# Optimization experiments

Hardware: AMD Instinct MI355X
Metric: run time of the kernel (lower is better)

Reference implementation:

```python
import jax, jax.numpy as jnp
import numpy as np

EPS_LN = 1e-5
EPS_ACT = 1e-5
EPS_W = 1e-8


def _layer_norm(x):
    # F.layer_norm(x, [d]) with no affine params, eps=1e-5, biased variance
    mu = jnp.mean(x, axis=-1, keepdims=True)
    xc = x - mu
    var = jnp.mean(xc * xc, axis=-1, keepdims=True)
    return xc * jax.lax.rsqrt(var + EPS_LN)


def _activation_quant(x):
    # per-token absmax int8 fake-quant (dequantized back to float)
    scale = 127.0 / jnp.clip(jnp.max(jnp.abs(x), axis=-1, keepdims=True), EPS_ACT)
    return jnp.clip(jnp.round(x * scale), -128, 127) / scale


def _weight_quant(w):
    # ternary {-1,0,+1} absmean quantization, rescaled by absmean
    scale = jnp.clip(jnp.mean(jnp.abs(w)), EPS_W)
    return jnp.clip(jnp.round(w / scale), -1, 1) * scale


def _bitlinear(x, w, b):
    xn = _layer_norm(x)
    xq = _activation_quant(xn)        # forward value (STE irrelevant for fwd)
    wq = _weight_quant(w)
    return jnp.einsum('bsd,fd->bsf', xq, wq) + b


def setup_inputs() -> dict:
    key = jax.random.key(0)
    k1, k2, k3, k4, k5 = jax.random.split(key, 5)
    d_model, d_ff = 2048, 8192
    B, S = 4, 2048
    x = jax.random.normal(k1, (B, S, d_model), dtype=jnp.float32)
    # nn.Linear default init: U(-1/sqrt(fan_in), 1/sqrt(fan_in))
    lim1 = 1.0 / np.sqrt(d_model)
    lim2 = 1.0 / np.sqrt(d_ff)
    w1 = jax.random.uniform(k2, (d_ff, d_model), jnp.float32, -lim1, lim1)
    b1 = jax.random.uniform(k3, (d_ff,), jnp.float32, -lim1, lim1)
    w2 = jax.random.uniform(k4, (d_model, d_ff), jnp.float32, -lim2, lim2)
    b2 = jax.random.uniform(k5, (d_model,), jnp.float32, -lim2, lim2)
    return {"x": x, "w1": w1, "b1": b1, "w2": w2, "b2": b2}


def reference(x, w1, b1, w2, b2):
    h = _bitlinear(x, w1, b1)
    h = jax.nn.gelu(h, approximate=False)  # torch F.gelu default = exact erf
    # dropout p=0.0 -> identity
    return _bitlinear(h, w2, b2)
```

## Files before the change

### kernel.cpp

```cpp
#include <hip/hip_runtime.h>

typedef int     i32x4 __attribute__((ext_vector_type(4)));
typedef _Float16 f16x2 __attribute__((ext_vector_type(2)));

__device__ __forceinline__ void async_cp16(const void* g, void* l) {
    __builtin_amdgcn_global_load_lds(
        (const __attribute__((address_space(1))) void*)g,
        (__attribute__((address_space(3))) void*)l, 16, 0, 0);
}

template <bool GELU, typename OutT>
__global__ __launch_bounds__(256) void gemm_i8(
    const signed char* __restrict__ A,
    const signed char* __restrict__ B,
    const float* __restrict__ rowinv,
    const float* __restrict__ wscale,
    const float* __restrict__ bias,
    OutT* __restrict__ C,
    int M, int N, int K)
{
    __shared__ signed char sA[128 * 128];
    __shared__ signed char sB[128 * 128];

    const int tid  = threadIdx.x;
    const int lane = tid & 63;
    const int wid  = tid >> 6;
    const int lm   = lane & 15;
    const int quad = lane >> 4;
    const int wr   = (wid >> 1) * 64;
    const int wc   = (wid & 1) * 64;

    const long long rowA0 = (long long)blockIdx.y * 128;
    const long long rowB0 = (long long)blockIdx.x * 128;

    const int srow   = tid >> 3;
    const int slot   = tid & 7;
    const int gchunk = slot ^ (srow & 7);

    const signed char* aP = A + (rowA0 + srow) * (long long)K + gchunk * 16;
    const signed char* bP = B + (rowB0 + srow) * (long long)K + gchunk * 16;
    signed char* sA_t = &sA[tid * 16];
    signed char* sB_t = &sB[tid * 16];
    const long long rstep = 32LL * K;

    i32x4 acc[4][4] = {};

    const int swz = lm & 7;

    for (int k0 = 0; k0 < K; k0 += 128) {
#pragma unroll
        for (int r = 0; r < 4; ++r) {
            async_cp16(aP + r * rstep + k0, sA_t + r * 4096);
            async_cp16(bP + r * rstep + k0, sB_t + r * 4096);
        }
        __syncthreads();
#pragma unroll
        for (int ks = 0; ks < 2; ++ks) {
            const int coff = ((ks * 4 + quad) ^ swz) * 16;
            i32x4 af[4], bfr[4];
#pragma unroll
            for (int i = 0; i < 4; ++i)
                af[i] = *(const i32x4*)&sA[(wr + i * 16 + lm) * 128 + coff];
#pragma unroll
            for (int j = 0; j < 4; ++j)
                bfr[j] = *(const i32x4*)&sB[(wc + j * 16 + lm) * 128 + coff];
#pragma unroll
            for (int i = 0; i < 4; ++i)
#pragma unroll
                for (int j = 0; j < 4; ++j)
                    acc[i][j] = __builtin_amdgcn_mfma_i32_16x16x64_i8(
                        af[i], bfr[j], acc[i][j], 0, 0, 0);
        }
        __syncthreads();
    }

    const float sw = wscale[0];
    float bj[4];
#pragma unroll
    for (int j = 0; j < 4; ++j)
        bj[j] = bias[rowB0 + wc + j * 16 + lm];

#pragma unroll
    for (int i = 0; i < 4; ++i) {
#pragma unroll
        for (int r = 0; r < 4; ++r) {
            const long long gr = rowA0 + wr + i * 16 + quad * 4 + r;
            const float rs = sw * rowinv[gr];
#pragma unroll
            for (int j = 0; j < 4; ++j) {
                const long long gc = rowB0 + wc + j * 16 + lm;
                float v = (float)acc[i][j][r] * rs + bj[j];
                if constexpr (GELU)
                    v = 0.5f * v * (1.0f + erff(v * 0.70710678118654752f));
                C[gr * (long long)N + gc] = (OutT)v;
            }
        }
    }
}

__global__ __launch_bounds__(256) void ln_quant_x(
    const float* __restrict__ x, signed char* __restrict__ xq,
    float* __restrict__ xinv)
{
    const int t = blockIdx.x;
    const int tid = threadIdx.x;
    const int lane = tid & 63, wid = tid >> 6;
    const float4* row = (const float4*)(x + (long long)t * 2048);
    float4 v0 = row[tid];
    float4 v1 = row[tid + 256];
    float vv[8] = {v0.x, v0.y, v0.z, v0.w, v1.x, v1.y, v1.z, v1.w};

    float s = 0.f, mn = vv[0], mx = vv[0];
#pragma unroll
    for (int i = 0; i < 8; ++i) { s += vv[i]; mn = fminf(mn, vv[i]); mx = fmaxf(mx, vv[i]); }
#pragma unroll
    for (int off = 32; off > 0; off >>= 1) {
        s += __shfl_down(s, off);
        mn = fminf(mn, __shfl_down(mn, off));
        mx = fmaxf(mx, __shfl_down(mx, off));
    }
    __shared__ float rS[4], rMn[4], rMx[4];
    if (lane == 0) { rS[wid] = s; rMn[wid] = mn; rMx[wid] = mx; }
    __syncthreads();
    s  = rS[0] + rS[1] + rS[2] + rS[3];
    mn = fminf(fminf(rMn[0], rMn[1]), fminf(rMn[2], rMn[3]));
    mx = fmaxf(fmaxf(rMx[0], rMx[1]), fmaxf(rMx[2], rMx[3]));
    const float mu = s * (1.0f / 2048.0f);

    float ssc = 0.f;
#pragma unroll
    for (int i = 0; i < 8; ++i) { float d = vv[i] - mu; ssc += d * d; }
#pragma unroll
    for (int off = 32; off > 0; off >>= 1) ssc += __shfl_down(ssc, off);
    __syncthreads();
    if (lane == 0) rS[wid] = ssc;
    __syncthreads();
    ssc = rS[0] + rS[1] + rS[2] + rS[3];

    const float var  = ssc * (1.0f / 2048.0f);
    const float rstd = 1.0f / sqrtf(var + 1e-5f);
    float am = fmaxf(mx - mu, mu - mn) * rstd;
    am = fmaxf(am, 1e-5f);
    const float scale = 127.0f / am;

    unsigned int b0 = 0, b1 = 0;
#pragma unroll
    for (int i = 0; i < 8; ++i) {
        float xn = (vv[i] - mu) * rstd;
        int qi = (int)fminf(fmaxf(rintf(xn * scale), -128.0f), 127.0f);
        unsigned int byte = (unsigned int)(qi & 0xff);
        if (i < 4) b0 |= byte << (i * 8);
        else       b1 |= byte << ((i - 4) * 8);
    }
    int* orow = (int*)(xq + (long long)t * 2048);
    orow[tid]       = (int)b0;
    orow[tid + 256] = (int)b1;
    if (tid == 0) xinv[t] = am / 127.0f;
}

__global__ __launch_bounds__(256) void ln_quant_h(
    const unsigned short* __restrict__ h, signed char* __restrict__ hq,
    float* __restrict__ hinv)
{
    const long long t = blockIdx.x;
    const int tid = threadIdx.x;
    const int lane = tid & 63, wid = tid >> 6;
    const unsigned short* row = h + t * 8192;

    uint4 raw[4];
    float v[32];
#pragma unroll
    for (int c = 0; c < 4; ++c) raw[c] = ((const uint4*)row)[c * 256 + tid];
#pragma unroll
    for (int c = 0; c < 4; ++c) {
        unsigned int u[4] = {raw[c].x, raw[c].y, raw[c].z, raw[c].w};
#pragma unroll
        for (int k = 0; k < 4; ++k) {
            f16x2 p = __builtin_bit_cast(f16x2, u[k]);
            v[c * 8 + k * 2 + 0] = (float)p[0];
            v[c * 8 + k * 2 + 1] = (float)p[1];
        }
    }

    float s = 0.f, mn = v[0], mx = v[0];
#pragma unroll
    for (int i = 0; i < 32; ++i) { s += v[i]; mn = fminf(mn, v[i]); mx = fmaxf(mx, v[i]); }
#pragma unroll
    for (int off = 32; off > 0; off >>= 1) {
        s += __shfl_down(s, off);
        mn = fminf(mn, __shfl_down(mn, off));
        mx = fmaxf(mx, __shfl_down(mx, off));
    }
    __shared__ float rS[4], rMn[4], rMx[4];
    if (lane == 0) { rS[wid] = s; rMn[wid] = mn; rMx[wid] = mx; }
    __syncthreads();
    s  = rS[0] + rS[1] + rS[2] + rS[3];
    mn = fminf(fminf(rMn[0], rMn[1]), fminf(rMn[2], rMn[3]));
    mx = fmaxf(fmaxf(rMx[0], rMx[1]), fmaxf(rMx[2], rMx[3]));
    const float mu = s * (1.0f / 8192.0f);

    float ssc = 0.f;
#pragma unroll
    for (int i = 0; i < 32; ++i) { float d = v[i] - mu; ssc += d * d; }
#pragma unroll
    for (int off = 32; off > 0; off >>= 1) ssc += __shfl_down(ssc, off);
    __syncthreads();
    if (lane == 0) rS[wid] = ssc;
    __syncthreads();
    ssc = rS[0] + rS[1] + rS[2] + rS[3];

    const float var  = ssc * (1.0f / 8192.0f);
    const float rstd = 1.0f / sqrtf(var + 1e-5f);
    float am = fmaxf(mx - mu, mu - mn) * rstd;
    am = fmaxf(am, 1e-5f);
    const float scale = 127.0f / am;

    signed char* orow = hq + t * 8192;
#pragma unroll
    for (int c = 0; c < 4; ++c) {
        unsigned int b0 = 0, b1 = 0;
#pragma unroll
        for (int k = 0; k < 8; ++k) {
            float xn = (v[c * 8 + k] - mu) * rstd;
            int qi = (int)fminf(fmaxf(rintf(xn * scale), -128.0f), 127.0f);
            unsigned int byte = (unsigned int)(qi & 0xff);
            if (k < 4) b0 |= byte << (k * 8);
            else       b1 |= byte << ((k - 4) * 8);
        }
        int2 o; o.x = (int)b0; o.y = (int)b1;
        ((int2*)orow)[c * 256 + tid] = o;
    }
    if (tid == 0) hinv[t] = am / 127.0f;
}

__global__ __launch_bounds__(256) void reduce_abs(
    const float4* __restrict__ w4, int n4, float* __restrict__ partial)
{
    const int tid = threadIdx.x;
    const int lane = tid & 63, wid = tid >> 6;
    float s = 0.f;
    for (int i = blockIdx.x * 256 + tid; i < n4; i += gridDim.x * 256) {
        float4 v = w4[i];
        s += fabsf(v.x) + fabsf(v.y) + fabsf(v.z) + fabsf(v.w);
    }
#pragma unroll
    for (int off = 32; off > 0; off >>= 1) s += __shfl_down(s, off);
    __shared__ float rS[4];
    if (lane == 0) rS[wid] = s;
    __syncthreads();
    if (tid == 0) partial[blockIdx.x] = rS[0] + rS[1] + rS[2] + rS[3];
}

__global__ __launch_bounds__(256) void finalize_scales(
    const float* __restrict__ p1, const float* __restrict__ p2,
    float* __restrict__ scales)
{
    const int tid = threadIdx.x;
    const int lane = tid & 63, wid = tid >> 6;
    float s1 = 0.f, s2 = 0.f;
    for (int i = tid; i < 1024; i += 256) { s1 += p1[i]; s2 += p2[i]; }
#pragma unroll
    for (int off = 32; off > 0; off >>= 1) {
        s1 += __shfl_down(s1, off);
        s2 += __shfl_down(s2, off);
    }
    __shared__ float rA[4], rB[4];
    if (lane == 0) { rA[wid] = s1; rB[wid] = s2; }
    __syncthreads();
    if (tid == 0) {
        float m1 = fmaxf((rA[0] + rA[1] + rA[2] + rA[3]) * (1.0f / 16777216.0f), 1e-8f);
        float m2 = fmaxf((rB[0] + rB[1] + rB[2] + rB[3]) * (1.0f / 16777216.0f), 1e-8f);
        scales[0] = m1;
        scales[1] = m2;
    }
}

__global__ __launch_bounds__(256) void quant_w(
    const float4* __restrict__ w4, signed char* __restrict__ wq,
    const float* __restrict__ scales, int sidx, int n4)
{
    const float s = scales[sidx];
    for (int i = blockIdx.x * 256 + threadIdx.x; i < n4; i += gridDim.x * 256) {
        float4 v = w4[i];
        int q0 = (int)fminf(fmaxf(rintf(v.x / s), -1.0f), 1.0f);
        int q1 = (int)fminf(fmaxf(rintf(v.y / s), -1.0f), 1.0f);
        int q2 = (int)fminf(fmaxf(rintf(v.z / s), -1.0f), 1.0f);
        int q3 = (int)fminf(fmaxf(rintf(v.w / s), -1.0f), 1.0f);
        unsigned int p = (unsigned int)(q0 & 0xff) | ((unsigned int)(q1 & 0xff) << 8)
                       | ((unsigned int)(q2 & 0xff) << 16) | ((unsigned int)(q3 & 0xff) << 24);
        ((unsigned int*)wq)[i] = p;
    }
}

extern "C" void kernel_launch(void* const* d_in, const int* in_sizes, int n_in,
                              void* d_out, int out_size, void* d_ws, size_t ws_size,
                              hipStream_t stream)
{
    const float* x  = (const float*)d_in[0];
    const float* w1 = (const float*)d_in[1];
    const float* b1 = (const float*)d_in[2];
    const float* w2 = (const float*)d_in[3];
    const float* b2 = (const float*)d_in[4];
    float* out = (float*)d_out;

    char* ws = (char*)d_ws;
    const size_t SZ_WQ = 16777216;
    signed char* w1q = (signed char*)(ws);
    signed char* w2q = (signed char*)(ws + SZ_WQ);
    signed char* xq  = (signed char*)(ws + 2 * SZ_WQ);
    unsigned short* h = (unsigned short*)(ws + 3 * SZ_WQ);
    signed char* hq  = (signed char*)(ws + 3 * SZ_WQ + 134217728);
    float* xinv   = (float*)(ws + 3 * SZ_WQ + 134217728 + 67108864);
    float* hinv   = xinv + 8192;
    float* part1  = hinv + 8192;
    float* part2  = part1 + 1024;
    float* scales = part2 + 1024;

    const int N4W = 4194304;

    reduce_abs<<<1024, 256, 0, stream>>>((const float4*)w1, N4W, part1);
    reduce_abs<<<1024, 256, 0, stream>>>((const float4*)w2, N4W, part2);
    finalize_scales<<<1, 256, 0, stream>>>(part1, part2, scales);
    quant_w<<<4096, 256, 0, stream>>>((const float4*)w1, w1q, scales, 0, N4W);
    quant_w<<<4096, 256, 0, stream>>>((const float4*)w2, w2q, scales, 1, N4W);
    ln_quant_x<<<8192, 256, 0, stream>>>(x, xq, xinv);

    gemm_i8<true, _Float16><<<dim3(64, 64), 256, 0, stream>>>(
        xq, w1q, xinv, &scales[0], b1, (_Float16*)h, 8192, 8192, 2048);

    ln_quant_h<<<8192, 256, 0, stream>>>(h, hq, hinv);

    gemm_i8<false, float><<<dim3(16, 64), 256, 0, stream>>>(
        hq, w2q, hinv, &scales[1], b2, out, 8192, 2048, 8192);
}
```

Baseline: 621.8 us.

## Replace int8 GEMM with 256x256 multi-stage pipelined 8-wave kernel

Replaces the single-buffered 128x128 int8 MFMA GEMM with a 256x256 tile kernel using 512 threads. It keeps four LDS stages with async global-to-LDS loads issued ahead, explicit waitcnt and barrier phases, and s_setprio around the MFMA bursts. It also adds an XCD-aware block remap and a new LDS swizzle. The goal is to hide global load latency behind compute and raise reuse per tile, at the cost of much higher LDS and register use, which limits occupancy.

```diff
diff --git a/kernel.cpp b/kernel.cpp
--- a/kernel.cpp
+++ b/kernel.cpp
@@ -1,6 +1,6 @@
 #include <hip/hip_runtime.h>
 
-typedef int     i32x4 __attribute__((ext_vector_type(4)));
+typedef int      i32x4 __attribute__((ext_vector_type(4)));
 typedef _Float16 f16x2 __attribute__((ext_vector_type(2)));
 
 __device__ __forceinline__ void async_cp16(const void* g, void* l) {
@@ -9,8 +9,41 @@
         (__attribute__((address_space(3))) void*)l, 16, 0, 0);
 }
 
+__device__ __forceinline__ void stage2(const signed char* base, long long o0,
+                                       long long o1, signed char* slab, int ldst) {
+    async_cp16(base + o0, slab + ldst);
+    async_cp16(base + o1, slab + 8192 + ldst);
+}
+
+__device__ __forceinline__ void rd_a4(const signed char* slab, int mh, int rowb, i32x4* af) {
+#pragma unroll
+    for (int i = 0; i < 4; ++i)
+        af[i] = *(const i32x4*)(slab + mh * 4096 + i * 1024 + rowb);
+}
+__device__ __forceinline__ void rd_b4(const signed char* slab, int rowb, i32x4* bf) {
+#pragma unroll
+    for (int j = 0; j < 4; ++j)
+        bf[j] = *(const i32x4*)(slab + j * 1024 + rowb);
+}
+__device__ __forceinline__ void mfma16(const i32x4* af, const i32x4* bf,
+                                       i32x4 acc[8][4], int mh) {
+#pragma unroll
+    for (int i = 0; i < 4; ++i)
+#pragma unroll
+        for (int j = 0; j < 4; ++j)
+            acc[mh * 4 + i][j] = __builtin_amdgcn_mfma_i32_16x16x64_i8(
+                af[i], bf[j], acc[mh * 4 + i][j], 0, 0, 0);
+}
+
+#define BAR  __builtin_amdgcn_s_barrier()
+#define LGKM0 do { asm volatile("s_waitcnt lgkmcnt(0)" ::: "memory"); \
+                   __builtin_amdgcn_sched_barrier(0); } while (0)
+#define VMW(N) do { asm volatile("s_waitcnt vmcnt(" #N ")" ::: "memory"); \
+                    __builtin_amdgcn_sched_barrier(0); } while (0)
+#define VMW_NONE do { } while (0)
+
 template <bool GELU, typename OutT>
-__global__ __launch_bounds__(256) void gemm_i8(
+__global__ __launch_bounds__(512, 2) void gemm_i8_8ph(
     const signed char* __restrict__ A,
     const signed char* __restrict__ B,
     const float* __restrict__ rowinv,
@@ -19,77 +52,116 @@
     OutT* __restrict__ C,
     int M, int N, int K)
 {
-    __shared__ signed char sA[128 * 128];
-    __shared__ signed char sB[128 * 128];
+    __shared__ signed char sA[4][16384];
+    __shared__ signed char sB[4][16384];
 
     const int tid  = threadIdx.x;
     const int lane = tid & 63;
     const int wid  = tid >> 6;
     const int lm   = lane & 15;
     const int quad = lane >> 4;
-    const int wr   = (wid >> 1) * 64;
-    const int wc   = (wid & 1) * 64;
-
-    const long long rowA0 = (long long)blockIdx.y * 128;
-    const long long rowB0 = (long long)blockIdx.x * 128;
-
-    const int srow   = tid >> 3;
-    const int slot   = tid & 7;
-    const int gchunk = slot ^ (srow & 7);
-
-    const signed char* aP = A + (rowA0 + srow) * (long long)K + gchunk * 16;
-    const signed char* bP = B + (rowB0 + srow) * (long long)K + gchunk * 16;
-    signed char* sA_t = &sA[tid * 16];
-    signed char* sB_t = &sB[tid * 16];
-    const long long rstep = 32LL * K;
-
-    i32x4 acc[4][4] = {};
-
-    const int swz = lm & 7;
-
-    for (int k0 = 0; k0 < K; k0 += 128) {
-#pragma unroll
-        for (int r = 0; r < 4; ++r) {
-            async_cp16(aP + r * rstep + k0, sA_t + r * 4096);
-            async_cp16(bP + r * rstep + k0, sB_t + r * 4096);
-        }
-        __syncthreads();
-#pragma unroll
-        for (int ks = 0; ks < 2; ++ks) {
-            const int coff = ((ks * 4 + quad) ^ swz) * 16;
-            i32x4 af[4], bfr[4];
-#pragma unroll
-            for (int i = 0; i < 4; ++i)
-                af[i] = *(const i32x4*)&sA[(wr + i * 16 + lm) * 128 + coff];
-#pragma unroll
-            for (int j = 0; j < 4; ++j)
-                bfr[j] = *(const i32x4*)&sB[(wc + j * 16 + lm) * 128 + coff];
-#pragma unroll
-            for (int i = 0; i < 4; ++i)
-#pragma unroll
-                for (int j = 0; j < 4; ++j)
-                    acc[i][j] = __builtin_amdgcn_mfma_i32_16x16x64_i8(
-                        af[i], bfr[j], acc[i][j], 0, 0, 0);
-        }
-        __syncthreads();
-    }
+    const int wm   = wid >> 2;
+    const int wn   = wid & 3;
+
+    const int nwg = gridDim.x * gridDim.y;
+    const int bid = blockIdx.y * gridDim.x + blockIdx.x;
+    const int cpx = nwg >> 3;
+    const int wg  = (bid & 7) * cpx + (bid >> 3);
+    const int bx  = wg % gridDim.x;
+    const int by  = wg / gridDim.x;
+
+    const long long rowA0 = (long long)by * 256;
+    const long long rowB0 = (long long)bx * 256;
+
+    const int srow   = tid >> 2;
+    const int schunk = (tid & 3) ^ ((tid >> 3) & 3);
+    const long long offA0 = (rowA0 + srow) * (long long)K + schunk * 16;
+    const long long offA1 = offA0 + 128LL * K;
+    const long long offB0 = (rowB0 + srow) * (long long)K + schunk * 16;
+    const long long offB1 = offB0 + 128LL * K;
+    const int ldst = tid * 16;
+
+    const int coff  = (quad ^ ((lm >> 1) & 3)) << 4;
+    const int rowbA = wm * 8192 + lm * 64 + coff;
+    const int rowbB = wn * 4096 + lm * 64 + coff;
+
+    const signed char* Ab = A;
+    const signed char* Bb = B;
+    const int NTt = K >> 7;
+
+    i32x4 acc[8][4] = {};
+
+#define TILE_BODY(T, DOA, DOB, VMA, VMB) do {                                   \
+        const int u0_ = 2 * (T);                                                \
+        const signed char* sa0_ = sA[u0_ & 3];                                  \
+        const signed char* sb0_ = sB[u0_ & 3];                                  \
+        const signed char* sa1_ = sA[(u0_ + 1) & 3];                            \
+        const signed char* sb1_ = sB[(u0_ + 1) & 3];                            \
+        i32x4 af[4], bf[4];                                                     \
+                                                        \
+        rd_a4(sa0_, 0, rowbA, af);                                              \
+        rd_b4(sb0_, rowbB, bf);                                                 \
+        if (DOA) stage2(Ab + (long long)(u0_ + 3) * 64, offA0, offA1,           \
+                        sA[(u0_ + 3) & 3], ldst);                               \
+        BAR; LGKM0;                                                             \
+        __builtin_amdgcn_s_setprio(1); mfma16(af, bf, acc, 0);                  \
+        __builtin_amdgcn_s_setprio(0);                                          \
+        BAR;                                                                    \
+                                             \
+        rd_a4(sa0_, 1, rowbA, af);                                              \
+        if (DOA) stage2(Bb + (long long)(u0_ + 3) * 64, offB0, offB1,           \
+                        sB[(u0_ + 3) & 3], ldst);                               \
+        BAR; LGKM0;                                                             \
+        __builtin_amdgcn_s_setprio(1); mfma16(af, bf, acc, 1);                  \
+        __builtin_amdgcn_s_setprio(0);                                          \
+        VMA; BAR;                                                               \
+                                                        \
+        rd_a4(sa1_, 0, rowbA, af);                                              \
+        rd_b4(sb1_, rowbB, bf);                                                 \
+        if (DOB) stage2(Ab + (long long)(u0_ + 4) * 64, offA0, offA1,           \
+                        sA[(u0_ + 4) & 3], ldst);                               \
+        BAR; LGKM0;                                                             \
+        __builtin_amdgcn_s_setprio(1); mfma16(af, bf, acc, 0);                  \
+        __builtin_amdgcn_s_setprio(0);                                          \
+        BAR;                                                                    \
+                                             \
+        rd_a4(sa1_, 1, rowbA, af);                                              \
+        if (DOB) stage2(Bb + (long long)(u0_ + 4) * 64, offB0, offB1,           \
+                        sB[(u0_ + 4) & 3], ldst);                               \
+        BAR; LGKM0;                                                             \
+        __builtin_amdgcn_s_setprio(1); mfma16(af, bf, acc, 1);                  \
+        __builtin_amdgcn_s_setprio(0);                                          \
+        VMB; BAR;                                                               \
+    } while (0)
+
+#pragma unroll
+    for (int u = 0; u < 3; ++u) {
+        stage2(Ab + (long long)u * 64, offA0, offA1, sA[u], ldst);
+        stage2(Bb + (long long)u * 64, offB0, offB1, sB[u], ldst);
+    }
+    VMW(8); BAR;
+
+    for (int t = 0; t < NTt - 2; ++t)
+        TILE_BODY(t, true, true, VMW(8), VMW(8));
+    TILE_BODY(NTt - 2, true, false, VMW(8), VMW(4));
+    TILE_BODY(NTt - 1, false, false, VMW(0), VMW_NONE);
+#undef TILE_BODY
 
     const float sw = wscale[0];
     float bj[4];
 #pragma unroll
     for (int j = 0; j < 4; ++j)
-        bj[j] = bias[rowB0 + wc + j * 16 + lm];
-
-#pragma unroll
-    for (int i = 0; i < 4; ++i) {
+        bj[j] = bias[rowB0 + wn * 64 + j * 16 + lm];
+#pragma unroll
+    for (int mi = 0; mi < 8; ++mi) {
 #pragma unroll
         for (int r = 0; r < 4; ++r) {
-            const long long gr = rowA0 + wr + i * 16 + quad * 4 + r;
+            const long long gr = rowA0 + wm * 128 + mi * 16 + quad * 4 + r;
             const float rs = sw * rowinv[gr];
 #pragma unroll
             for (int j = 0; j < 4; ++j) {
-                const long long gc = rowB0 + wc + j * 16 + lm;
-                float v = (float)acc[i][j][r] * rs + bj[j];
+                const long long gc = rowB0 + wn * 64 + j * 16 + lm;
+                float v = (float)acc[mi][j][r] * rs + bj[j];
                 if constexpr (GELU)
                     v = 0.5f * v * (1.0f + erff(v * 0.70710678118654752f));
                 C[gr * (long long)N + gc] = (OutT)v;
@@ -325,11 +397,11 @@
     quant_w<<<4096, 256, 0, stream>>>((const float4*)w2, w2q, scales, 1, N4W);
     ln_quant_x<<<8192, 256, 0, stream>>>(x, xq, xinv);
 
-    gemm_i8<true, _Float16><<<dim3(64, 64), 256, 0, stream>>>(
+    gemm_i8_8ph<true, _Float16><<<dim3(32, 32), 512, 0, stream>>>(
         xq, w1q, xinv, &scales[0], b1, (_Float16*)h, 8192, 8192, 2048);
 
     ln_quant_h<<<8192, 256, 0, stream>>>(h, hq, hinv);
 
-    gemm_i8<false, float><<<dim3(16, 64), 256, 0, stream>>>(
+    gemm_i8_8ph<false, float><<<dim3(8, 32), 512, 0, stream>>>(
         hq, w2q, hinv, &scales[1], b2, out, 8192, 2048, 8192);
 }
```

After: 598.1 us. 1.04x faster.

## Rewrite int8 GEMM with 256x256 tiles, 32x32 MFMA and 4-stage async pipeline

Applied to the files above, without the earlier changes.

Replaces the 128x128 single-buffered int8 GEMM with a 512-thread kernel computing 256x256 tiles. It uses 32x32x32 int8 MFMA instructions and a 4-slot LDS ring of 64-wide K slabs, prefetching three slabs ahead under explicit vmcnt/lgkmcnt waits and raised MFMA priority. It also remaps block IDs so that consecutive workgroups are spread across XCDs. The aim is to hide global-load latency and raise reuse per LDS byte. The cost is 128KB of LDS per block and hand-written wait counts that must exactly match the number of outstanding loads.

```diff
diff --git a/kernel.cpp b/kernel.cpp
--- a/kernel.cpp
+++ b/kernel.cpp
@@ -1,7 +1,8 @@
 #include <hip/hip_runtime.h>
 
-typedef int     i32x4 __attribute__((ext_vector_type(4)));
-typedef _Float16 f16x2 __attribute__((ext_vector_type(2)));
+typedef int      i32x4  __attribute__((ext_vector_type(4)));
+typedef int      i32x16 __attribute__((ext_vector_type(16)));
+typedef _Float16 f16x2  __attribute__((ext_vector_type(2)));
 
 __device__ __forceinline__ void async_cp16(const void* g, void* l) {
     __builtin_amdgcn_global_load_lds(
@@ -9,8 +10,47 @@
         (__attribute__((address_space(3))) void*)l, 16, 0, 0);
 }
 
+__device__ __forceinline__ void stage2(const signed char* g0, const signed char* g1,
+                                       signed char* slab, int ldst) {
+    async_cp16(g0, slab + ldst);
+    async_cp16(g1, slab + 8192 + ldst);
+}
+
+__device__ __forceinline__ void rd_frags(const signed char* sa, const signed char* sb,
+                                         int aoff0, int aoff1, int boff0, int boff1,
+                                         i32x4 af[4][2], i32x4 bf[2][2]) {
+#pragma unroll
+    for (int mb = 0; mb < 4; ++mb) {
+        af[mb][0] = *(const i32x4*)(sa + mb * 2048 + aoff0);
+        af[mb][1] = *(const i32x4*)(sa + mb * 2048 + aoff1);
+    }
+#pragma unroll
+    for (int nb = 0; nb < 2; ++nb) {
+        bf[nb][0] = *(const i32x4*)(sb + nb * 2048 + boff0);
+        bf[nb][1] = *(const i32x4*)(sb + nb * 2048 + boff1);
+    }
+}
+
+__device__ __forceinline__ void mfma16x(const i32x4 af[4][2], const i32x4 bf[2][2],
+                                        i32x16 acc[4][2]) {
+#pragma unroll
+    for (int ks = 0; ks < 2; ++ks)
+#pragma unroll
+        for (int mb = 0; mb < 4; ++mb)
+#pragma unroll
+            for (int nb = 0; nb < 2; ++nb)
+                acc[mb][nb] = __builtin_amdgcn_mfma_i32_32x32x32_i8(
+                    af[mb][ks], bf[nb][ks], acc[mb][nb], 0, 0, 0);
+}
+
+#define LGKM0 do { asm volatile("s_waitcnt lgkmcnt(0)" ::: "memory"); \
+                   __builtin_amdgcn_sched_barrier(0); } while (0)
+#define VMW(N) do { asm volatile("s_waitcnt vmcnt(" #N ")" ::: "memory"); \
+                    __builtin_amdgcn_sched_barrier(0); } while (0)
+#define GNONE do { } while (0)
+
 template <bool GELU, typename OutT>
-__global__ __launch_bounds__(256) void gemm_i8(
+__global__ __launch_bounds__(512, 2) void gemm_i8_32(
     const signed char* __restrict__ A,
     const signed char* __restrict__ B,
     const float* __restrict__ rowinv,
@@ -19,77 +59,95 @@
     OutT* __restrict__ C,
     int M, int N, int K)
 {
-    __shared__ signed char sA[128 * 128];
-    __shared__ signed char sB[128 * 128];
+    __shared__ signed char sA[4][16384];
+    __shared__ signed char sB[4][16384];
 
     const int tid  = threadIdx.x;
     const int lane = tid & 63;
     const int wid  = tid >> 6;
-    const int lm   = lane & 15;
-    const int quad = lane >> 4;
-    const int wr   = (wid >> 1) * 64;
-    const int wc   = (wid & 1) * 64;
-
-    const long long rowA0 = (long long)blockIdx.y * 128;
-    const long long rowB0 = (long long)blockIdx.x * 128;
-
-    const int srow   = tid >> 3;
-    const int slot   = tid & 7;
-    const int gchunk = slot ^ (srow & 7);
-
-    const signed char* aP = A + (rowA0 + srow) * (long long)K + gchunk * 16;
-    const signed char* bP = B + (rowB0 + srow) * (long long)K + gchunk * 16;
-    signed char* sA_t = &sA[tid * 16];
-    signed char* sB_t = &sB[tid * 16];
-    const long long rstep = 32LL * K;
-
-    i32x4 acc[4][4] = {};
-
-    const int swz = lm & 7;
-
-    for (int k0 = 0; k0 < K; k0 += 128) {
-#pragma unroll
-        for (int r = 0; r < 4; ++r) {
-            async_cp16(aP + r * rstep + k0, sA_t + r * 4096);
-            async_cp16(bP + r * rstep + k0, sB_t + r * 4096);
-        }
-        __syncthreads();
-#pragma unroll
-        for (int ks = 0; ks < 2; ++ks) {
-            const int coff = ((ks * 4 + quad) ^ swz) * 16;
-            i32x4 af[4], bfr[4];
-#pragma unroll
-            for (int i = 0; i < 4; ++i)
-                af[i] = *(const i32x4*)&sA[(wr + i * 16 + lm) * 128 + coff];
-#pragma unroll
-            for (int j = 0; j < 4; ++j)
-                bfr[j] = *(const i32x4*)&sB[(wc + j * 16 + lm) * 128 + coff];
-#pragma unroll
-            for (int i = 0; i < 4; ++i)
-#pragma unroll
-                for (int j = 0; j < 4; ++j)
-                    acc[i][j] = __builtin_amdgcn_mfma_i32_16x16x64_i8(
-                        af[i], bfr[j], acc[i][j], 0, 0, 0);
-        }
-        __syncthreads();
-    }
+    const int wm   = wid >> 2;
+    const int wn   = wid & 3;
+
+    const int nwg = gridDim.x * gridDim.y;
+    const int bid = blockIdx.y * gridDim.x + blockIdx.x;
+    const int cpx = nwg >> 3;
+    const int wg  = (bid & 7) * cpx + (bid >> 3);
+    const int bx  = wg % gridDim.x;
+    const int by  = wg / gridDim.x;
+
+    const long long rowA0 = (long long)by * 256;
+    const long long rowB0 = (long long)bx * 256;
+
+    const int srow   = tid >> 2;
+    const int schunk = (tid & 3) ^ ((tid >> 3) & 3);
+    const signed char* aG0 = A + (rowA0 + srow) * (long long)K + schunk * 16;
+    const signed char* aG1 = aG0 + 128LL * K;
+    const signed char* bG0 = B + (rowB0 + srow) * (long long)K + schunk * 16;
+    const signed char* bG1 = bG0 + 128LL * K;
+    const int ldst = tid * 16;
+
+    const int r32 = lane & 31;
+    const int kc  = lane >> 5;
+    const int swz = (r32 >> 1) & 3;
+    const int sl0 = ((0 * 2 + kc) ^ swz) << 4;
+    const int sl1 = ((1 * 2 + kc) ^ swz) << 4;
+    const int aoff0 = wm * 8192 + r32 * 64 + sl0;
+    const int aoff1 = wm * 8192 + r32 * 64 + sl1;
+    const int boff0 = wn * 4096 + r32 * 64 + sl0;
+    const int boff1 = wn * 4096 + r32 * 64 + sl1;
+
+    const int NTt = K >> 7;
+
+    i32x16 acc[4][2] = {};
+    i32x4 af[4][2], bf[2][2];
+
+#define PH(SL, DOST, KOFF, GATE) do {                                          \
+        rd_frags(sA[SL], sB[SL], aoff0, aoff1, boff0, boff1, af, bf);          \
+        if (DOST) {                                                            \
+            stage2(aG0 + (KOFF), aG1 + (KOFF), sA[(SL + 3) & 3], ldst);        \
+            stage2(bG0 + (KOFF), bG1 + (KOFF), sB[(SL + 3) & 3], ldst);        \
+        }                                                                      \
+        __builtin_amdgcn_s_barrier(); LGKM0;                                   \
+        __builtin_amdgcn_s_setprio(1); mfma16x(af, bf, acc);                   \
+        __builtin_amdgcn_s_setprio(0);                                         \
+        GATE; __builtin_amdgcn_s_barrier();                                    \
+    } while (0)
+
+    stage2(aG0,       aG1,       sA[0], ldst); stage2(bG0,       bG1,       sB[0], ldst);
+    stage2(aG0 + 64,  aG1 + 64,  sA[1], ldst); stage2(bG0 + 64,  bG1 + 64,  sB[1], ldst);
+    stage2(aG0 + 128, aG1 + 128, sA[2], ldst); stage2(bG0 + 128, bG1 + 128, sB[2], ldst);
+    VMW(8); __builtin_amdgcn_s_barrier();
+
+    int koff = 192;
+    for (int t = 0; t < NTt - 2; t += 2) {
+        PH(0, true, koff,       VMW(8));
+        PH(1, true, koff + 64,  VMW(8));
+        PH(2, true, koff + 128, VMW(8));
+        PH(3, true, koff + 192, VMW(8));
+        koff += 256;
+    }
+    PH(0, true,  koff, VMW(8));
+    PH(1, false, 0,    VMW(4));
+    PH(2, false, 0,    VMW(0));
+    PH(3, false, 0,    GNONE);
+#undef PH
 
     const float sw = wscale[0];
-    float bj[4];
-#pragma unroll
-    for (int j = 0; j < 4; ++j)
-        bj[j] = bias[rowB0 + wc + j * 16 + lm];
-
-#pragma unroll
-    for (int i = 0; i < 4; ++i) {
-#pragma unroll
-        for (int r = 0; r < 4; ++r) {
-            const long long gr = rowA0 + wr + i * 16 + quad * 4 + r;
+    float bjv[2];
+#pragma unroll
+    for (int nb = 0; nb < 2; ++nb)
+        bjv[nb] = bias[rowB0 + wn * 64 + nb * 32 + r32];
+#pragma unroll
+    for (int mb = 0; mb < 4; ++mb) {
+#pragma unroll
+        for (int r = 0; r < 16; ++r) {
+            const int lrow = (r & 3) + 8 * (r >> 2) + 4 * kc;
+            const long long gr = rowA0 + wm * 128 + mb * 32 + lrow;
             const float rs = sw * rowinv[gr];
 #pragma unroll
-            for (int j = 0; j < 4; ++j) {
-                const long long gc = rowB0 + wc + j * 16 + lm;
-                float v = (float)acc[i][j][r] * rs + bj[j];
+            for (int nb = 0; nb < 2; ++nb) {
+                const long long gc = rowB0 + wn * 64 + nb * 32 + r32;
+                float v = (float)acc[mb][nb][r] * rs + bjv[nb];
                 if constexpr (GELU)
                     v = 0.5f * v * (1.0f + erff(v * 0.70710678118654752f));
                 C[gr * (long long)N + gc] = (OutT)v;
@@ -325,11 +383,11 @@
     quant_w<<<4096, 256, 0, stream>>>((const float4*)w2, w2q, scales, 1, N4W);
     ln_quant_x<<<8192, 256, 0, stream>>>(x, xq, xinv);
 
-    gemm_i8<true, _Float16><<<dim3(64, 64), 256, 0, stream>>>(
+    gemm_i8_32<true, _Float16><<<dim3(32, 32), 512, 0, stream>>>(
         xq, w1q, xinv, &scales[0], b1, (_Float16*)h, 8192, 8192, 2048);
 
     ln_quant_h<<<8192, 256, 0, stream>>>(h, hq, hinv);
 
-    gemm_i8<false, float><<<dim3(16, 64), 256, 0, stream>>>(
+    gemm_i8_32<false, float><<<dim3(8, 32), 512, 0, stream>>>(
         hq, w2q, hinv, &scales[1], b2, out, 8192, 2048, 8192);
 }
```

Measured after the change: 619.5 us. Within noise of the previous version (-0.4%).
